# Performance work log

Measured on AMD Instinct MI355X. Metric: run time of the kernel, lower is better.

The kernel has to match this reference:

```python
import jax, jax.numpy as jnp
import numpy as np

NB = 50  # nb_steps
IN_D = 64
HID = 128
B = 256


def _cc_weights(nb):
    # Faithful port of UMNN compute_cc_weights (Clenshaw-Curtis quadrature)
    lam = np.arange(0, nb + 1).reshape(-1, 1).astype(np.float64)
    lam = np.cos((lam @ lam.T) * np.pi / nb)
    lam[:, 0] = 0.5
    lam[:, -1] = 0.5 * lam[:, -1]
    lam = lam * 2.0 / nb
    W = np.arange(0, nb + 1).reshape(-1, 1).astype(np.float64)
    W[np.arange(1, nb + 1, 2)] = 0
    W = 2.0 / (1.0 - W ** 2)
    W[0] = 1
    W[np.arange(1, nb + 1, 2)] = 0
    cc = (lam.T @ W)[:, 0].astype(np.float32)              # [nb+1]
    steps = np.cos(np.arange(0, nb + 1) * np.pi / nb).astype(np.float32)  # [nb+1]
    return jnp.asarray(cc), jnp.asarray(steps)


def setup_inputs() -> dict:
    key = jax.random.key(0)
    ks = jax.random.split(key, 16)
    d = {}
    d["x"] = jax.random.normal(ks[0], (B, 1), dtype=jnp.float32)
    d["h"] = jax.random.normal(ks[1], (B, IN_D - 1), dtype=jnp.float32)

    def lin(kw, kb, fan_in, fan_out):
        s = 1.0 / np.sqrt(fan_in)
        w = jax.random.uniform(kw, (fan_in, fan_out), jnp.float32, -s, s)
        b = jax.random.uniform(kb, (fan_out,), jnp.float32, -s, s)
        return w, b

    # Integrand MLP: in_d -> 128 -> 128 -> 1
    d["iw0"], d["ib0"] = lin(ks[2], ks[3], IN_D, HID)
    d["iw1"], d["ib1"] = lin(ks[4], ks[5], HID, HID)
    d["iw2"], d["ib2"] = lin(ks[6], ks[7], HID, 1)
    # Outer net: (in_d-1) -> 128 -> 128 -> 2
    d["nw0"], d["nb0"] = lin(ks[8], ks[9], IN_D - 1, HID)
    d["nw1"], d["nb1"] = lin(ks[10], ks[11], HID, HID)
    d["nw2"], d["nb2"] = lin(ks[12], ks[13], HID, 2)
    return d


def reference(x, h, iw0, ib0, iw1, ib1, iw2, ib2, nw0, nb0, nw1, nb1, nw2, nb2):
    cc, steps = _cc_weights(NB)  # [S1], [S1]
    S1 = NB + 1
    b = x.shape[0]

    # ----- outer quadrature: integral over t in [0, x] -----
    # t[b, i] = 0 + (x - 0) * (steps[i] + 1) / 2
    t = x[:, None, :] * (steps[None, :, None] + 1.0) / 2.0          # [B, S1, 1]

    # ----- inner UMNN: integral over s in [t, xmax], xmax = max(t) + 10 -----
    xmax = jnp.max(t) + 10.0
    s = t[:, :, None, :] + (xmax - t)[:, :, None, :] * (steps[None, None, :, None] + 1.0) / 2.0  # [B,S1,S1,1]

    hb = jnp.broadcast_to(h[:, None, None, :], (b, S1, S1, h.shape[1]))
    inp = jnp.concatenate([s, hb], axis=-1)                         # [B,S1,S1,in_d]

    # PostiveIntegrandNN: Lin-ReLU-Lin-ReLU-Lin-ELU, then + 1.0
    a = jax.nn.relu(inp @ iw0 + ib0)
    a = jax.nn.relu(a @ iw1 + ib1)
    f = jax.nn.elu(a @ iw2 + ib2) + 1.0                              # [B,S1,S1,1]

    # inner Clenshaw-Curtis reduction: z * (xT - x0) / 2
    inner = jnp.sum(f * cc[None, None, :, None], axis=2) * (xmax - t) / 2.0   # [B,S1,1]

    # outer reduction: integral from 0 to x
    outer = jnp.sum(inner * cc[None, :, None], axis=1) * x / 2.0    # [B,1]

    # outer dense net on h -> offset / scaling
    o = jax.nn.relu(h @ nw0 + nb0)
    o = jax.nn.relu(o @ nw1 + nb1)
    o = o @ nw2 + nb2                                               # [B,2]
    offset = o[:, 0:1]
    scaling = jnp.exp(o[:, 1:2])
    return scaling * outer + offset
```

## Files before the change

### kernel.cpp

```cpp
#include <hip/hip_runtime.h>
#include <math.h>

#define NBQ 50
#define S1 51
#define NPTS 2601
#define NTILES 163
#define IN_D 64
#define HID 128
#define BSZ 256
#define NCHUNK 4
#define NUMAX 41

typedef __bf16 bf16x8 __attribute__((ext_vector_type(8)));
typedef float  f32x4  __attribute__((ext_vector_type(4)));

#define WS_CC     0
#define WS_STEPS  64
#define WS_XMAX   128
#define WS_BASE   256
#define WS_SCAL   33024
#define WS_OFF    33280
#define WS_PART   33536
#define WS_W1BF   41728

__global__ void k_prep(const float* __restrict__ x, const float* __restrict__ h,
                       const float* __restrict__ iw0, const float* __restrict__ ib0,
                       const float* __restrict__ iw1,
                       const float* __restrict__ nw0, const float* __restrict__ nb0,
                       const float* __restrict__ nw1, const float* __restrict__ nb1,
                       const float* __restrict__ nw2, const float* __restrict__ nb2,
                       float* __restrict__ ws) {
    int blk = blockIdx.x;
    int tid = threadIdx.x;

    if (blk < 64) {
        int idx  = blk * 256 + tid;
        int e    = idx & 7;
        int lane = (idx >> 3) & 63;
        int fk   = idx >> 9;
        int kk   = fk & 3;
        int nt   = fk >> 2;
        int k = kk * 32 + (lane >> 4) * 8 + e;
        int n = nt * 16 + (lane & 15);
        __bf16* w1bf = (__bf16*)(ws + WS_W1BF);
        w1bf[idx] = (__bf16)iw1[k * HID + n];
        return;
    }

    __shared__ float s_steps[S1];
    __shared__ float s_red[4];
    __shared__ float s_h[IN_D - 1];
    __shared__ float s_o0[HID];
    __shared__ float s_part[4];

    if (blk == 64) {
        int t = tid;
        if (t < S1) {
            double st = cos((double)t * M_PI / (double)NBQ);
            s_steps[t] = (float)st;
            ws[WS_STEPS + t] = (float)st;
            double acc = 0.0;
            for (int i = 0; i <= NBQ; ++i) {
                double Wi;
                if (i == 0)       Wi = 1.0;
                else if (i & 1)   Wi = 0.0;
                else              Wi = 2.0 / (1.0 - (double)i * (double)i);
                double lam;
                if (t == 0)  lam = 0.5;
                else         lam = cos((double)i * (double)t * M_PI / (double)NBQ);
                if (t == NBQ) lam *= 0.5;
                lam *= 2.0 / (double)NBQ;
                acc += lam * Wi;
            }
            ws[WS_CC + t] = (float)acc;
        }
        __syncthreads();
        float xb = x[t];
        float m = -1e30f;
        for (int i = 0; i < S1; ++i)
            m = fmaxf(m, xb * (s_steps[i] + 1.0f) * 0.5f);
        for (int off = 32; off > 0; off >>= 1)
            m = fmaxf(m, __shfl_down(m, off));
        if ((t & 63) == 0) s_red[t >> 6] = m;
        __syncthreads();
        if (t == 0) {
            float mm = fmaxf(fmaxf(s_red[0], s_red[1]), fmaxf(s_red[2], s_red[3]));
            ws[WS_XMAX] = mm + 10.0f;
        }
        return;
    }

    int b = blk - 65;
    int n = tid;
    bool act = (n < HID);
    if (act && n < IN_D - 1) s_h[n] = h[b * (IN_D - 1) + n];
    __syncthreads();
    float o1 = 0.0f;
    if (act) {
        float accB = ib0[n];
        float acc0 = nb0[n];
        for (int d = 0; d < IN_D - 1; ++d) {
            float hv = s_h[d];
            accB = fmaf(hv, iw0[(1 + d) * HID + n], accB);
            acc0 = fmaf(hv, nw0[d * HID + n], acc0);
        }
        ws[WS_BASE + b * HID + n] = accB;
        s_o0[n] = fmaxf(acc0, 0.0f);
    }
    __syncthreads();
    if (act) {
        float acc1 = nb1[n];
        for (int m = 0; m < HID; ++m)
            acc1 = fmaf(s_o0[m], nw1[m * HID + n], acc1);
        o1 = fmaxf(acc1, 0.0f);
    }
    float p0 = act ? o1 * nw2[n * 2 + 0] : 0.0f;
    float p1 = act ? o1 * nw2[n * 2 + 1] : 0.0f;
    for (int off = 32; off > 0; off >>= 1) {
        p0 += __shfl_down(p0, off);
        p1 += __shfl_down(p1, off);
    }
    int lane = tid & 63, w = tid >> 6;
    if (lane == 0 && w < 2) { s_part[w * 2] = p0; s_part[w * 2 + 1] = p1; }
    __syncthreads();
    if (tid == 0) {
        ws[WS_OFF + b]  = s_part[0] + s_part[2] + nb2[0];
        ws[WS_SCAL + b] = expf(s_part[1] + s_part[3] + nb2[1]);
    }
}

__global__ __launch_bounds__(256, 4) void k3_mfma(
        const float* __restrict__ x,
        const float* __restrict__ iw0,
        const float* __restrict__ ib1,
        const float* __restrict__ iw2,
        const float* __restrict__ ib2,
        float* __restrict__ ws) {
    __shared__ bf16x8 bfr_lds[4][4][64];
    __shared__ float zlds[4][NUMAX][17];
    __shared__ float s_tbl[NUMAX][16];
    __shared__ float w_tbl[NUMAX][16];

    int blk  = blockIdx.x;
    int b    = blk >> 2;
    int c    = blk & 3;
    int tid  = threadIdx.x;
    int wave = tid >> 6;
    int lane = tid & 63;
    int col  = lane & 15;
    int g    = lane >> 4;

    float xmax = ws[WS_XMAX];
    float xb   = x[b];
    float b2   = ib2[0];

    int NU = (c < 3) ? 41 : 40;
    int G  = (NU + 3) >> 2;

    for (int e = tid; e < NU * 16; e += 256) {
        int u  = e >> 4;
        int cl = e & 15;
        int p  = (c + 4 * u) * 16 + cl;
        int pc = (p < NPTS) ? p : (NPTS - 1);
        int i  = (int)(((unsigned)pc * 10281u) >> 19);
        int j  = pc - i * 51;
        float sti = ws[WS_STEPS + i];
        float stj = ws[WS_STEPS + j];
        float ti  = xb * (sti + 1.0f) * 0.5f;
        float w   = xmax - ti;
        s_tbl[u][cl] = fmaf(w, (stj + 1.0f) * 0.5f, ti);
        w_tbl[u][cl] = ws[WS_CC + i] * ws[WS_CC + j] * w;
    }

    const bf16x8* w1f = (const bf16x8*)(ws + WS_W1BF);
    bf16x8 Af[2][4];
#pragma unroll
    for (int nt = 0; nt < 2; ++nt) {
        int NT = wave * 2 + nt;
#pragma unroll
        for (int kk = 0; kk < 4; ++kk)
            Af[nt][kk] = w1f[(NT * 4 + kk) * 64 + lane];
    }

    const float* basep = ws + WS_BASE + b * HID;
    int m0 = wave * 32 + g * 8;
    f32x4 w0a = *(const f32x4*)(iw0 + m0);
    f32x4 w0b = *(const f32x4*)(iw0 + m0 + 4);
    f32x4 bsa = *(const f32x4*)(basep + m0);
    f32x4 bsb = *(const f32x4*)(basep + m0 + 4);

    f32x4 accInit[2], iw2v[2];
#pragma unroll
    for (int nt = 0; nt < 2; ++nt) {
        int n0 = (wave * 2 + nt) * 16 + g * 4;
        accInit[nt] = *(const f32x4*)(ib1 + n0);
        iw2v[nt]    = *(const f32x4*)(iw2 + n0);
    }

    __syncthreads();

    for (int grp = 0; grp < G; ++grp) {
        int ubase = grp * 4;
#pragma unroll
        for (int t = 0; t < 4; ++t) {
            int u = ubase + t;
            if (u < NU) {
                float s = s_tbl[u][col];
                bf16x8 bfr;
#pragma unroll
                for (int e = 0; e < 4; ++e) {
                    bfr[e]     = (__bf16)fmaxf(fmaf(s, w0a[e], bsa[e]), 0.0f);
                    bfr[4 + e] = (__bf16)fmaxf(fmaf(s, w0b[e], bsb[e]), 0.0f);
                }
                bfr_lds[t][wave][lane] = bfr;
            }
        }
        __syncthreads();
#pragma unroll
        for (int t = 0; t < 4; ++t) {
            int u = ubase + t;
            if (u < NU) {
                bf16x8 f0 = bfr_lds[t][0][lane];
                bf16x8 f1 = bfr_lds[t][1][lane];
                bf16x8 f2 = bfr_lds[t][2][lane];
                bf16x8 f3 = bfr_lds[t][3][lane];
                f32x4 a0 = __builtin_amdgcn_mfma_f32_16x16x32_bf16(Af[0][0], f0, accInit[0], 0, 0, 0);
                f32x4 a1 = __builtin_amdgcn_mfma_f32_16x16x32_bf16(Af[1][0], f0, accInit[1], 0, 0, 0);
                a0 = __builtin_amdgcn_mfma_f32_16x16x32_bf16(Af[0][1], f1, a0, 0, 0, 0);
                a1 = __builtin_amdgcn_mfma_f32_16x16x32_bf16(Af[1][1], f1, a1, 0, 0, 0);
                a0 = __builtin_amdgcn_mfma_f32_16x16x32_bf16(Af[0][2], f2, a0, 0, 0, 0);
                a1 = __builtin_amdgcn_mfma_f32_16x16x32_bf16(Af[1][2], f2, a1, 0, 0, 0);
                a0 = __builtin_amdgcn_mfma_f32_16x16x32_bf16(Af[0][3], f3, a0, 0, 0, 0);
                a1 = __builtin_amdgcn_mfma_f32_16x16x32_bf16(Af[1][3], f3, a1, 0, 0, 0);

                float za = 0.f, zb = 0.f;
#pragma unroll
                for (int q = 0; q < 4; ++q) {
                    za = fmaf(fmaxf(a0[q], 0.0f), iw2v[0][q], za);
                    zb = fmaf(fmaxf(a1[q], 0.0f), iw2v[1][q], zb);
                }
                float z = za + zb;
                z += __shfl_xor(z, 16);
                z += __shfl_xor(z, 32);
                if (lane < 16) zlds[wave][u][lane] = z;
            }
        }
        __syncthreads();
    }

    float vsum = 0.0f;
    int npass = (NU + 15) >> 4;
    for (int pass = 0; pass < npass; ++pass) {
        int u = pass * 16 + wave * 4 + g;
        if (u < NU) {
            int p = (c + 4 * u) * 16 + col;
            if (p < NPTS) {
                float z = zlds[0][u][col] + zlds[1][u][col]
                        + zlds[2][u][col] + zlds[3][u][col] + b2;
                float f = (z > 0.0f) ? (z + 1.0f) : __expf(z);
                vsum += w_tbl[u][col] * f;
            }
        }
    }
#pragma unroll
    for (int off = 1; off < 64; off <<= 1)
        vsum += __shfl_xor(vsum, off);
    if (lane == 0)
        ws[WS_PART + blk * 4 + wave] = vsum * 0.5f;
}

__global__ void k4_final(const float* __restrict__ x, const float* __restrict__ ws,
                         float* __restrict__ out) {
    int b = threadIdx.x;
    float sum = 0.0f;
#pragma unroll
    for (int c = 0; c < 16; ++c) sum += ws[WS_PART + b * 16 + c];
    out[b] = ws[WS_SCAL + b] * sum * x[b] * 0.5f + ws[WS_OFF + b];
}

extern "C" void kernel_launch(void* const* d_in, const int* in_sizes, int n_in,
                              void* d_out, int out_size, void* d_ws, size_t ws_size,
                              hipStream_t stream) {
    const float* x   = (const float*)d_in[0];
    const float* h   = (const float*)d_in[1];
    const float* iw0 = (const float*)d_in[2];
    const float* ib0 = (const float*)d_in[3];
    const float* iw1 = (const float*)d_in[4];
    const float* ib1 = (const float*)d_in[5];
    const float* iw2 = (const float*)d_in[6];
    const float* ib2 = (const float*)d_in[7];
    const float* nw0 = (const float*)d_in[8];
    const float* nb0 = (const float*)d_in[9];
    const float* nw1 = (const float*)d_in[10];
    const float* nb1 = (const float*)d_in[11];
    const float* nw2 = (const float*)d_in[12];
    const float* nb2 = (const float*)d_in[13];
    float* ws  = (float*)d_ws;
    float* out = (float*)d_out;

    hipLaunchKernelGGL(k_prep, dim3(64 + 1 + BSZ), dim3(256), 0, stream,
                       x, h, iw0, ib0, iw1, nw0, nb0, nw1, nb1, nw2, nb2, ws);
    hipLaunchKernelGGL(k3_mfma, dim3(BSZ * NCHUNK), dim3(256), 0, stream,
                       x, iw0, ib1, iw2, ib2, ws);
    hipLaunchKernelGGL(k4_final, dim3(1), dim3(BSZ), 0, stream, x, ws, out);
}
```

Before: 49.84 us.

## Halve k3 block to two waves each owning four N-tiles; use packed bf16 convert

The MFMA kernel now runs 128 threads per block, with each wave owning four 16-column output tiles instead of two. Each wave builds two K-slices of the layer-0 activations and issues sixteen MFMAs per point group. The activation conversion now uses an inline v_cvt_pk_bf16_f32 to pack pairs of floats. The aim is to halve the cross-wave z partials and reduction work and to give each wave more independent MFMA chains, at the cost of more registers per thread and fewer waves per block for latency hiding.

Measured after the change: 51.40 us. +3.1%, slower.

```diff
diff --git a/kernel.cpp b/kernel.cpp
--- a/kernel.cpp
+++ b/kernel.cpp
@@ -4,7 +4,6 @@
 #define NBQ 50
 #define S1 51
 #define NPTS 2601
-#define NTILES 163
 #define IN_D 64
 #define HID 128
 #define BSZ 256
@@ -13,6 +12,7 @@
 
 typedef __bf16 bf16x8 __attribute__((ext_vector_type(8)));
 typedef float  f32x4  __attribute__((ext_vector_type(4)));
+typedef unsigned int u32x4 __attribute__((ext_vector_type(4)));
 
 #define WS_CC     0
 #define WS_STEPS  64
@@ -22,6 +22,12 @@
 #define WS_OFF    33280
 #define WS_PART   33536
 #define WS_W1BF   41728
+
+static __device__ inline unsigned int cvt_pk_bf16(float lo, float hi) {
+    unsigned int r;
+    asm("v_cvt_pk_bf16_f32 %0, %1, %2" : "=v"(r) : "v"(lo), "v"(hi));
+    return r;
+}
 
 __global__ void k_prep(const float* __restrict__ x, const float* __restrict__ h,
                        const float* __restrict__ iw0, const float* __restrict__ ib0,
@@ -129,7 +135,7 @@
     }
 }
 
-__global__ __launch_bounds__(256, 4) void k3_mfma(
+__global__ __launch_bounds__(128, 2) void k3_mfma(
         const float* __restrict__ x,
         const float* __restrict__ iw0,
         const float* __restrict__ ib1,
@@ -137,9 +143,10 @@
         const float* __restrict__ ib2,
         float* __restrict__ ws) {
     __shared__ bf16x8 bfr_lds[4][4][64];
-    __shared__ float zlds[4][NUMAX][17];
+    __shared__ float zlds[2][NUMAX][17];
     __shared__ float s_tbl[NUMAX][16];
     __shared__ float w_tbl[NUMAX][16];
+    __shared__ float s_red[2];
 
     int blk  = blockIdx.x;
     int b    = blk >> 2;
@@ -157,7 +164,7 @@
     int NU = (c < 3) ? 41 : 40;
     int G  = (NU + 3) >> 2;
 
-    for (int e = tid; e < NU * 16; e += 256) {
+    for (int e = tid; e < NU * 16; e += 128) {
         int u  = e >> 4;
         int cl = e & 15;
         int p  = (c + 4 * u) * 16 + cl;
@@ -173,26 +180,32 @@
     }
 
     const bf16x8* w1f = (const bf16x8*)(ws + WS_W1BF);
-    bf16x8 Af[2][4];
-#pragma unroll
-    for (int nt = 0; nt < 2; ++nt) {
-        int NT = wave * 2 + nt;
+    bf16x8 Af[4][4];
+#pragma unroll
+    for (int nt = 0; nt < 4; ++nt) {
+        int NT = wave * 4 + nt;
 #pragma unroll
         for (int kk = 0; kk < 4; ++kk)
             Af[nt][kk] = w1f[(NT * 4 + kk) * 64 + lane];
     }
 
     const float* basep = ws + WS_BASE + b * HID;
-    int m0 = wave * 32 + g * 8;
-    f32x4 w0a = *(const f32x4*)(iw0 + m0);
-    f32x4 w0b = *(const f32x4*)(iw0 + m0 + 4);
-    f32x4 bsa = *(const f32x4*)(basep + m0);
-    f32x4 bsb = *(const f32x4*)(basep + m0 + 4);
-
-    f32x4 accInit[2], iw2v[2];
-#pragma unroll
-    for (int nt = 0; nt < 2; ++nt) {
-        int n0 = (wave * 2 + nt) * 16 + g * 4;
+    int kk0 = wave * 2;
+    int mA = kk0 * 32 + g * 8;
+    int mB = mA + 32;
+    f32x4 w0A0 = *(const f32x4*)(iw0 + mA);
+    f32x4 w0A1 = *(const f32x4*)(iw0 + mA + 4);
+    f32x4 bsA0 = *(const f32x4*)(basep + mA);
+    f32x4 bsA1 = *(const f32x4*)(basep + mA + 4);
+    f32x4 w0B0 = *(const f32x4*)(iw0 + mB);
+    f32x4 w0B1 = *(const f32x4*)(iw0 + mB + 4);
+    f32x4 bsB0 = *(const f32x4*)(basep + mB);
+    f32x4 bsB1 = *(const f32x4*)(basep + mB + 4);
+
+    f32x4 accInit[4], iw2v[4];
+#pragma unroll
+    for (int nt = 0; nt < 4; ++nt) {
+        int n0 = (wave * 4 + nt) * 16 + g * 4;
         accInit[nt] = *(const f32x4*)(ib1 + n0);
         iw2v[nt]    = *(const f32x4*)(iw2 + n0);
     }
@@ -206,13 +219,37 @@
             int u = ubase + t;
             if (u < NU) {
                 float s = s_tbl[u][col];
-                bf16x8 bfr;
-#pragma unroll
-                for (int e = 0; e < 4; ++e) {
-                    bfr[e]     = (__bf16)fmaxf(fmaf(s, w0a[e], bsa[e]), 0.0f);
-                    bfr[4 + e] = (__bf16)fmaxf(fmaf(s, w0b[e], bsb[e]), 0.0f);
+                u32x4 pkA, pkB;
+                {
+                    float v0 = fmaxf(fmaf(s, w0A0[0], bsA0[0]), 0.0f);
+                    float v1 = fmaxf(fmaf(s, w0A0[1], bsA0[1]), 0.0f);
+                    float v2 = fmaxf(fmaf(s, w0A0[2], bsA0[2]), 0.0f);
+                    float v3 = fmaxf(fmaf(s, w0A0[3], bsA0[3]), 0.0f);
+                    float v4 = fmaxf(fmaf(s, w0A1[0], bsA1[0]), 0.0f);
+                    float v5 = fmaxf(fmaf(s, w0A1[1], bsA1[1]), 0.0f);
+                    float v6 = fmaxf(fmaf(s, w0A1[2], bsA1[2]), 0.0f);
+                    float v7 = fmaxf(fmaf(s, w0A1[3], bsA1[3]), 0.0f);
+                    pkA[0] = cvt_pk_bf16(v0, v1);
+                    pkA[1] = cvt_pk_bf16(v2, v3);
+                    pkA[2] = cvt_pk_bf16(v4, v5);
+                    pkA[3] = cvt_pk_bf16(v6, v7);
                 }
-                bfr_lds[t][wave][lane] = bfr;
+                {
+                    float v0 = fmaxf(fmaf(s, w0B0[0], bsB0[0]), 0.0f);
+                    float v1 = fmaxf(fmaf(s, w0B0[1], bsB0[1]), 0.0f);
+                    float v2 = fmaxf(fmaf(s, w0B0[2], bsB0[2]), 0.0f);
+                    float v3 = fmaxf(fmaf(s, w0B0[3], bsB0[3]), 0.0f);
+                    float v4 = fmaxf(fmaf(s, w0B1[0], bsB1[0]), 0.0f);
+                    float v5 = fmaxf(fmaf(s, w0B1[1], bsB1[1]), 0.0f);
+                    float v6 = fmaxf(fmaf(s, w0B1[2], bsB1[2]), 0.0f);
+                    float v7 = fmaxf(fmaf(s, w0B1[3], bsB1[3]), 0.0f);
+                    pkB[0] = cvt_pk_bf16(v0, v1);
+                    pkB[1] = cvt_pk_bf16(v2, v3);
+                    pkB[2] = cvt_pk_bf16(v4, v5);
+                    pkB[3] = cvt_pk_bf16(v6, v7);
+                }
+                bfr_lds[t][kk0][lane]     = __builtin_bit_cast(bf16x8, pkA);
+                bfr_lds[t][kk0 + 1][lane] = __builtin_bit_cast(bf16x8, pkB);
             }
         }
         __syncthreads();
@@ -224,20 +261,27 @@
                 bf16x8 f1 = bfr_lds[t][1][lane];
                 bf16x8 f2 = bfr_lds[t][2][lane];
                 bf16x8 f3 = bfr_lds[t][3][lane];
-                f32x4 a0 = __builtin_amdgcn_mfma_f32_16x16x32_bf16(Af[0][0], f0, accInit[0], 0, 0, 0);
-                f32x4 a1 = __builtin_amdgcn_mfma_f32_16x16x32_bf16(Af[1][0], f0, accInit[1], 0, 0, 0);
-                a0 = __builtin_amdgcn_mfma_f32_16x16x32_bf16(Af[0][1], f1, a0, 0, 0, 0);
-                a1 = __builtin_amdgcn_mfma_f32_16x16x32_bf16(Af[1][1], f1, a1, 0, 0, 0);
-                a0 = __builtin_amdgcn_mfma_f32_16x16x32_bf16(Af[0][2], f2, a0, 0, 0, 0);
-                a1 = __builtin_amdgcn_mfma_f32_16x16x32_bf16(Af[1][2], f2, a1, 0, 0, 0);
-                a0 = __builtin_amdgcn_mfma_f32_16x16x32_bf16(Af[0][3], f3, a0, 0, 0, 0);
-                a1 = __builtin_amdgcn_mfma_f32_16x16x32_bf16(Af[1][3], f3, a1, 0, 0, 0);
+                f32x4 acc[4];
+#pragma unroll
+                for (int nt = 0; nt < 4; ++nt)
+                    acc[nt] = __builtin_amdgcn_mfma_f32_16x16x32_bf16(Af[nt][0], f0, accInit[nt], 0, 0, 0);
+#pragma unroll
+                for (int nt = 0; nt < 4; ++nt)
+                    acc[nt] = __builtin_amdgcn_mfma_f32_16x16x32_bf16(Af[nt][1], f1, acc[nt], 0, 0, 0);
+#pragma unroll
+                for (int nt = 0; nt < 4; ++nt)
+                    acc[nt] = __builtin_amdgcn_mfma_f32_16x16x32_bf16(Af[nt][2], f2, acc[nt], 0, 0, 0);
+#pragma unroll
+                for (int nt = 0; nt < 4; ++nt)
+                    acc[nt] = __builtin_amdgcn_mfma_f32_16x16x32_bf16(Af[nt][3], f3, acc[nt], 0, 0, 0);
 
                 float za = 0.f, zb = 0.f;
 #pragma unroll
                 for (int q = 0; q < 4; ++q) {
-                    za = fmaf(fmaxf(a0[q], 0.0f), iw2v[0][q], za);
-                    zb = fmaf(fmaxf(a1[q], 0.0f), iw2v[1][q], zb);
+                    za = fmaf(fmaxf(acc[0][q], 0.0f), iw2v[0][q], za);
+                    zb = fmaf(fmaxf(acc[1][q], 0.0f), iw2v[1][q], zb);
+                    za = fmaf(fmaxf(acc[2][q], 0.0f), iw2v[2][q], za);
+                    zb = fmaf(fmaxf(acc[3][q], 0.0f), iw2v[3][q], zb);
                 }
                 float z = za + zb;
                 z += __shfl_xor(z, 16);
@@ -249,14 +293,13 @@
     }
 
     float vsum = 0.0f;
-    int npass = (NU + 15) >> 4;
+    int npass = (NU + 7) >> 3;
     for (int pass = 0; pass < npass; ++pass) {
-        int u = pass * 16 + wave * 4 + g;
+        int u = pass * 8 + wave * 4 + g;
         if (u < NU) {
             int p = (c + 4 * u) * 16 + col;
             if (p < NPTS) {
-                float z = zlds[0][u][col] + zlds[1][u][col]
-                        + zlds[2][u][col] + zlds[3][u][col] + b2;
+                float z = zlds[0][u][col] + zlds[1][u][col] + b2;
                 float f = (z > 0.0f) ? (z + 1.0f) : __expf(z);
                 vsum += w_tbl[u][col] * f;
             }
@@ -265,8 +308,10 @@
 #pragma unroll
     for (int off = 1; off < 64; off <<= 1)
         vsum += __shfl_xor(vsum, off);
-    if (lane == 0)
-        ws[WS_PART + blk * 4 + wave] = vsum * 0.5f;
+    if (lane == 0) s_red[wave] = vsum;
+    __syncthreads();
+    if (tid == 0)
+        ws[WS_PART + blk] = (s_red[0] + s_red[1]) * 0.5f;
 }
 
 __global__ void k4_final(const float* __restrict__ x, const float* __restrict__ ws,
@@ -274,7 +319,7 @@
     int b = threadIdx.x;
     float sum = 0.0f;
 #pragma unroll
-    for (int c = 0; c < 16; ++c) sum += ws[WS_PART + b * 16 + c];
+    for (int c = 0; c < 4; ++c) sum += ws[WS_PART + b * 4 + c];
     out[b] = ws[WS_SCAL + b] * sum * x[b] * 0.5f + ws[WS_OFF + b];
 }
 
@@ -300,7 +345,7 @@
 
     hipLaunchKernelGGL(k_prep, dim3(64 + 1 + BSZ), dim3(256), 0, stream,
                        x, h, iw0, ib0, iw1, nw0, nb0, nw1, nb1, nw2, nb2, ws);
-    hipLaunchKernelGGL(k3_mfma, dim3(BSZ * NCHUNK), dim3(256), 0, stream,
+    hipLaunchKernelGGL(k3_mfma, dim3(BSZ * NCHUNK), dim3(128), 0, stream,
                        x, iw0, ib1, iw2, ib2, ws);
     hipLaunchKernelGGL(k4_final, dim3(1), dim3(BSZ), 0, stream, x, ws, out);
 }
```
